# Kernel optimization log

Hardware: AMD Instinct MI355X
Metric: run time of the kernel (lower is better)

## Reference

```python
import jax, jax.numpy as jnp
import numpy as np

N, E = 50000, 1_600_000
IN, HID, OUT = 2048, 64, 64


def setup_inputs() -> dict:
    key = jax.random.key(0)
    k1, k2, k3, k4 = jax.random.split(key, 4)
    x = jax.random.normal(k1, (N, IN), dtype=jnp.float32)
    edge_index = jax.random.randint(k2, (2, E), 0, N, dtype=jnp.int64)
    W1 = jax.random.normal(k3, (IN, HID), dtype=jnp.float32) / np.sqrt(IN)
    b1 = jnp.zeros((HID,), dtype=jnp.float32)
    W2 = jax.random.normal(k4, (HID, OUT), dtype=jnp.float32) / np.sqrt(HID)
    b2 = jnp.zeros((OUT,), dtype=jnp.float32)
    return {"x": x, "edge_index": edge_index, "W1": W1, "b1": b1, "W2": W2, "b2": b2}


def gcn_conv(x, edge_index, W, b):
    # PyG GCNConv: h = XW; out = D^{-1/2} (A + I) D^{-1/2} h + b
    n = x.shape[0]
    h = x @ W  # [n, d_out]
    loops = jnp.arange(n, dtype=edge_index.dtype)
    src = jnp.concatenate([edge_index[0], loops])  # [E+n]
    dst = jnp.concatenate([edge_index[1], loops])
    deg = jax.ops.segment_sum(jnp.ones_like(dst, dtype=h.dtype), dst, num_segments=n)
    dinv = jax.lax.rsqrt(deg)  # deg >= 1 because of self-loops
    norm = dinv[src] * dinv[dst]  # [E+n]
    out = jax.ops.segment_sum(h[src] * norm[:, None], dst, num_segments=n)
    return out + b


def reference(x, edge_index, W1, b1, W2, b2):
    h = jax.nn.relu(gcn_conv(x, edge_index, W1, b1))
    h = jax.nn.relu(gcn_conv(h, edge_index, W2, b2))
    return h.mean(axis=0)  # [OUT]
```

## Files before the change

kernel.cpp:

```cpp
#include <hip/hip_runtime.h>
#include <hip/hip_bf16.h>

typedef __attribute__((ext_vector_type(8))) short short8_t;
typedef __attribute__((ext_vector_type(4))) float f32x4;

__device__ __forceinline__ short f2bf(float x){
  union { float f; unsigned u; } v; v.f = x;
  unsigned r = v.u + 0x7fffu + ((v.u >> 16) & 1u);
  return (short)(r >> 16);
}
__device__ __forceinline__ unsigned pack2(float lo, float hi){
  return (unsigned)(unsigned short)f2bf(lo) | ((unsigned)(unsigned short)f2bf(hi) << 16);
}
__device__ __forceinline__ float bf2f(unsigned short u){
  union { unsigned u; float f; } v; v.u = ((unsigned)u) << 16; return v.f;
}

__global__ __launch_bounds__(256) void k_wconv2(const float* __restrict__ W1, short* __restrict__ Wb1,
                                                const float* __restrict__ W2, short* __restrict__ Wb2){
  int tid = blockIdx.x*256 + threadIdx.x;
  const float* W; short* Wb; int t;
  if (tid < 64*2048){ W = W1; Wb = Wb1; t = tid; }
  else if (tid < 64*2048 + 2*2048){ W = W2; Wb = Wb2; t = tid - 64*2048; }
  else return;
  int e  = t & 7;
  int l  = (t >> 3) & 63;
  int nt = (t >> 9) & 3;
  int kt = t >> 11;
  int k  = kt*32 + (l >> 4)*8 + e;
  int col = nt*16 + (l & 15);
  Wb[t] = f2bf(W[(size_t)k*64 + col]);
}

__global__ __launch_bounds__(256) void k_hist_gemm1(const int* __restrict__ ei, int* __restrict__ cnt,
                                                    int* __restrict__ rank, int E,
                                                    const float* __restrict__ A, const short* __restrict__ Wb,
                                                    float* __restrict__ h1raw, int M, int EB){
  __shared__ unsigned short lds[64*256];
  if ((int)blockIdx.x < EB){
    int i = blockIdx.x*256 + threadIdx.x;
    if (i < E) rank[i] = atomicAdd(&cnt[ei[E + i]], 1);
    return;
  }
  int wid = threadIdx.x >> 6, lane = threadIdx.x & 63;
  int row0 = (blockIdx.x - EB)*64 + wid*16;
  if (row0 >= M) return;
  int rfrag = lane & 15, g = lane >> 4;
  char* ldsb = (char*)lds;
  const short8_t* wb = (const short8_t*)Wb + lane;
  f32x4 acc0 = {0.f,0.f,0.f,0.f}, acc1 = acc0, acc2 = acc0, acc3 = acc0;

  int wbase = wid*16*512;
  int wsel  = (lane >> 1);
  int whalf = (lane & 1) << 3;

  for (int ko = 0; ko < 8; ++ko){
    #pragma unroll
    for (int r = 0; r < 16; ++r){
      const float4 a = *(const float4*)(A + (size_t)(row0 + r)*2048 + ko*256 + lane*4);
      uint2 p; p.x = pack2(a.x, a.y); p.y = pack2(a.z, a.w);
      *(uint2*)(ldsb + wbase + r*512 + ((wsel ^ (r & 7)) << 4) + whalf) = p;
    }
    asm volatile("s_waitcnt lgkmcnt(0)" ::: "memory");
    #pragma unroll
    for (int kt = 0; kt < 8; ++kt){
      short8_t af = *(const short8_t*)(ldsb + wbase + rfrag*512 + ((((kt<<2) + g) ^ (rfrag & 7)) << 4));
      int ktg = ko*8 + kt;
      short8_t b0 = wb[(ktg*4+0)*64];
      short8_t b1 = wb[(ktg*4+1)*64];
      short8_t b2 = wb[(ktg*4+2)*64];
      short8_t b3 = wb[(ktg*4+3)*64];
      acc0 = __builtin_amdgcn_mfma_f32_16x16x32_bf16(af, b0, acc0, 0,0,0);
      acc1 = __builtin_amdgcn_mfma_f32_16x16x32_bf16(af, b1, acc1, 0,0,0);
      acc2 = __builtin_amdgcn_mfma_f32_16x16x32_bf16(af, b2, acc2, 0,0,0);
      acc3 = __builtin_amdgcn_mfma_f32_16x16x32_bf16(af, b3, acc3, 0,0,0);
    }
  }

  int orow = row0 + g*4;
  float* op = h1raw + (size_t)orow*64 + rfrag;
  #pragma unroll
  for (int reg = 0; reg < 4; ++reg){
    op[reg*64 +  0] = acc0[reg];
    op[reg*64 + 16] = acc1[reg];
    op[reg*64 + 32] = acc2[reg];
    op[reg*64 + 48] = acc3[reg];
  }
}

__global__ __launch_bounds__(256) void k_part(const int* __restrict__ cnt, int* __restrict__ partial, int N){
  int b = blockIdx.x, t = threadIdx.x;
  int chunk = (N + 255) >> 8;
  int lo = b*chunk, hi = lo + chunk; if (hi > N) hi = N;
  int s = 0;
  for (int i = lo + t; i < hi; i += 256) s += cnt[i];
  __shared__ int sm[256];
  sm[t] = s; __syncthreads();
  for (int d = 128; d; d >>= 1){ if (t < d) sm[t] += sm[t+d]; __syncthreads(); }
  if (t == 0) partial[b] = sm[0];
}

__global__ __launch_bounds__(256) void k_scan2(const int* __restrict__ cnt, const int* __restrict__ partial,
                                               int* __restrict__ off, float* __restrict__ dinv, int N){
  int b = blockIdx.x, t = threadIdx.x;
  __shared__ int ps[256];
  ps[t] = partial[t]; __syncthreads();
  for (int d = 1; d < 256; d <<= 1){
    int v = (t >= d) ? ps[t-d] : 0; __syncthreads(); ps[t] += v; __syncthreads();
  }
  int base  = b ? ps[b-1] : 0;
  int total = ps[255];
  int chunk = (N + 255) >> 8;
  int lo = b*chunk, hi = lo + chunk; if (hi > N) hi = N;
  __shared__ int vs[256];
  int run = base;
  for (int j0 = lo; j0 < hi; j0 += 256){
    int i = j0 + t;
    int c = (i < hi) ? cnt[i] : 0;
    vs[t] = c; __syncthreads();
    for (int d = 1; d < 256; d <<= 1){
      int v = (t >= d) ? vs[t-d] : 0; __syncthreads(); vs[t] += v; __syncthreads();
    }
    if (i < hi){
      off[i] = run + vs[t] - c;
      dinv[i] = rsqrtf((float)(c + 1));
    }
    run += vs[255];
    __syncthreads();
  }
  if (b == 255 && t == 0) off[N] = total;
}

__global__ __launch_bounds__(256) void k_scatter_scale(const int* __restrict__ ei, const int* __restrict__ off,
                                                       const int* __restrict__ rank, int* __restrict__ ebuf, int E,
                                                       const float* __restrict__ h1raw, const float* __restrict__ dinv,
                                                       unsigned short* __restrict__ h1, int total8, int EB){
  if ((int)blockIdx.x < EB){
    int i = blockIdx.x*256 + threadIdx.x;
    if (i < E){
      int s = ei[i], d = ei[E + i];
      ebuf[off[d] + rank[i]] = s;
    }
    return;
  }
  int t = (blockIdx.x - EB)*256 + threadIdx.x;
  if (t >= total8) return;
  int base = t*8;
  float dv = dinv[base >> 6];
  const float4 a0 = *(const float4*)(h1raw + base);
  const float4 a1 = *(const float4*)(h1raw + base + 4);
  short8_t o;
  o[0]=f2bf(a0.x*dv); o[1]=f2bf(a0.y*dv); o[2]=f2bf(a0.z*dv); o[3]=f2bf(a0.w*dv);
  o[4]=f2bf(a1.x*dv); o[5]=f2bf(a1.y*dv); o[6]=f2bf(a1.z*dv); o[7]=f2bf(a1.w*dv);
  *(short8_t*)(h1 + base) = o;
}

template<int KTILES>
__global__ __launch_bounds__(256) void k_gemm_sm(const unsigned short* __restrict__ Ah,
                                                 const short* __restrict__ Wb, const float* __restrict__ dinv,
                                                 unsigned short* __restrict__ out, int M, int lda){
  int wid = threadIdx.x >> 6, lane = threadIdx.x & 63;
  int row0 = (blockIdx.x*4 + wid)*16;
  if (row0 >= M) return;
  int r = lane & 15, g = lane >> 4;
  const short8_t* wb = (const short8_t*)Wb + lane;
  f32x4 acc0 = {0.f,0.f,0.f,0.f}, acc1 = acc0, acc2 = acc0, acc3 = acc0;
  #pragma unroll
  for (int kt = 0; kt < KTILES; ++kt){
    short8_t af = *(const short8_t*)(Ah + (size_t)(row0 + r)*lda + kt*32 + g*8);
    short8_t b0 = wb[(kt*4+0)*64];
    short8_t b1 = wb[(kt*4+1)*64];
    short8_t b2 = wb[(kt*4+2)*64];
    short8_t b3 = wb[(kt*4+3)*64];
    acc0 = __builtin_amdgcn_mfma_f32_16x16x32_bf16(af, b0, acc0, 0,0,0);
    acc1 = __builtin_amdgcn_mfma_f32_16x16x32_bf16(af, b1, acc1, 0,0,0);
    acc2 = __builtin_amdgcn_mfma_f32_16x16x32_bf16(af, b2, acc2, 0,0,0);
    acc3 = __builtin_amdgcn_mfma_f32_16x16x32_bf16(af, b3, acc3, 0,0,0);
  }
  int orow = row0 + g*4;
  float d0 = dinv[orow], d1 = dinv[orow+1], d2 = dinv[orow+2], d3 = dinv[orow+3];
  unsigned short* op = out + (size_t)orow*64 + r;
  op[0*64 +  0] = (unsigned short)f2bf(acc0[0]*d0);
  op[0*64 + 16] = (unsigned short)f2bf(acc1[0]*d0);
  op[0*64 + 32] = (unsigned short)f2bf(acc2[0]*d0);
  op[0*64 + 48] = (unsigned short)f2bf(acc3[0]*d0);
  op[1*64 +  0] = (unsigned short)f2bf(acc0[1]*d1);
  op[1*64 + 16] = (unsigned short)f2bf(acc1[1]*d1);
  op[1*64 + 32] = (unsigned short)f2bf(acc2[1]*d1);
  op[1*64 + 48] = (unsigned short)f2bf(acc3[1]*d1);
  op[2*64 +  0] = (unsigned short)f2bf(acc0[2]*d2);
  op[2*64 + 16] = (unsigned short)f2bf(acc1[2]*d2);
  op[2*64 + 32] = (unsigned short)f2bf(acc2[2]*d2);
  op[2*64 + 48] = (unsigned short)f2bf(acc3[2]*d2);
  op[3*64 +  0] = (unsigned short)f2bf(acc0[3]*d3);
  op[3*64 + 16] = (unsigned short)f2bf(acc1[3]*d3);
  op[3*64 + 32] = (unsigned short)f2bf(acc2[3]*d3);
  op[3*64 + 48] = (unsigned short)f2bf(acc3[3]*d3);
}

template<bool FUSE>
__global__ __launch_bounds__(256) void k_agg(const unsigned short* __restrict__ hin, const int* __restrict__ off,
                                             const int* __restrict__ ebuf, const float* __restrict__ dinv,
                                             const float* __restrict__ bias, void* __restrict__ outp, int N){
  int lane = threadIdx.x & 63, wid = threadIdx.x >> 6;
  float b = bias[lane];
  float fsum = 0.f;
  int stride = gridDim.x*4;
  for (int i = blockIdx.x*4 + wid; i < N; i += stride){
    float acc = bf2f(hin[(size_t)i*64 + lane]);
    int j  = off[i];
    int j1 = off[i+1];
    for (; j + 4 <= j1; j += 4){
      int s0 = ebuf[j], s1 = ebuf[j+1], s2 = ebuf[j+2], s3 = ebuf[j+3];
      acc += bf2f(hin[(size_t)s0*64 + lane]);
      acc += bf2f(hin[(size_t)s1*64 + lane]);
      acc += bf2f(hin[(size_t)s2*64 + lane]);
      acc += bf2f(hin[(size_t)s3*64 + lane]);
    }
    for (; j < j1; ++j){
      int s = ebuf[j];
      acc += bf2f(hin[(size_t)s*64 + lane]);
    }
    float z = fmaxf(dinv[i]*acc + b, 0.f);
    if (FUSE) fsum += z;
    else ((unsigned short*)outp)[(size_t)i*64 + lane] = (unsigned short)f2bf(z);
  }
  if (FUSE){
    __shared__ float sm[4][64];
    sm[wid][lane] = fsum;
    __syncthreads();
    if (wid == 0)
      ((float*)outp)[(size_t)blockIdx.x*64 + lane] = sm[0][lane] + sm[1][lane] + sm[2][lane] + sm[3][lane];
  }
}

__global__ __launch_bounds__(256) void k_final(const float* __restrict__ part, float* __restrict__ out,
                                               int NB, float invN){
  int f = blockIdx.x;
  float s = 0.f;
  for (int b = threadIdx.x; b < NB; b += 256) s += part[(size_t)b*64 + f];
  __shared__ float sm[256];
  sm[threadIdx.x] = s; __syncthreads();
  for (int d = 128; d > 0; d >>= 1){
    if (threadIdx.x < d) sm[threadIdx.x] += sm[threadIdx.x + d];
    __syncthreads();
  }
  if (threadIdx.x == 0) out[f] = sm[0]*invN;
}

extern "C" void kernel_launch(void* const* d_in, const int* in_sizes, int n_in,
                              void* d_out, int out_size, void* d_ws, size_t ws_size,
                              hipStream_t stream){
  const float* x  = (const float*)d_in[0];
  const int*   ei = (const int*)d_in[1];
  const float* W1 = (const float*)d_in[2];
  const float* b1 = (const float*)d_in[3];
  const float* W2 = (const float*)d_in[4];
  const float* b2 = (const float*)d_in[5];
  float* out = (float*)d_out;

  const int IN = 2048;
  int N = in_sizes[0] / IN;
  int E = in_sizes[1] / 2;

  char* w = (char*)d_ws;
  auto alloc = [&](size_t bytes){ char* p = w; w += (bytes + 255) & ~255ULL; return (void*)p; };
  int*   cnt     = (int*)  alloc((size_t)N*4);
  int*   off     = (int*)  alloc((size_t)(N+1)*4);
  float* dinv    = (float*)alloc((size_t)N*4);
  int*   partial = (int*)  alloc(256*4);
  int*   rank    = (int*)  alloc((size_t)E*4);
  int*   ebuf    = (int*)  alloc((size_t)E*4);
  short* Wb1     = (short*)alloc((size_t)64*2048*2);
  short* Wb2     = (short*)alloc((size_t)2*2048*2);
  float* h1raw   = (float*)alloc((size_t)N*64*4);
  unsigned short* h1 = (unsigned short*)alloc((size_t)N*64*2);
  unsigned short* z1 = (unsigned short*)alloc((size_t)N*64*2);
  const int NB2 = 2048;
  float* part    = (float*)alloc((size_t)NB2*64*4);

  int EB = (E + 255)/256;
  int GB = (N + 63)/64;
  int total8 = N*8;
  int SB = (total8 + 255)/256;
  int smblocks = ((N + 15)/16 + 3)/4;

  hipMemsetAsync(cnt, 0, (size_t)N*4, stream);
  k_wconv2 <<<(64*2048 + 2*2048 + 255)/256, 256, 0, stream>>>(W1, Wb1, W2, Wb2);
  k_hist_gemm1<<<EB + GB, 256, 0, stream>>>(ei, cnt, rank, E, x, Wb1, h1raw, N, EB);
  k_part   <<<256, 256, 0, stream>>>(cnt, partial, N);
  k_scan2  <<<256, 256, 0, stream>>>(cnt, partial, off, dinv, N);
  k_scatter_scale<<<EB + SB, 256, 0, stream>>>(ei, off, rank, ebuf, E, h1raw, dinv, h1, total8, EB);
  k_agg<false><<<NB2, 256, 0, stream>>>(h1, off, ebuf, dinv, b1, (void*)z1, N);
  k_gemm_sm<2><<<smblocks, 256, 0, stream>>>(z1, Wb2, dinv, h1, N, 64);
  k_agg<true> <<<NB2, 256, 0, stream>>>(h1, off, ebuf, dinv, b2, (void*)part, N);
  k_final  <<<64, 256, 0, stream>>>(part, out, NB2, 1.0f/(float)N);
}
```

Before: 366.6 us.

## Split GEMM1 K across wave pairs, interleave histogram blocks, use packed bf16 convert

```diff
diff --git a/kernel.cpp b/kernel.cpp
--- a/kernel.cpp
+++ b/kernel.cpp
@@ -9,8 +9,10 @@
   unsigned r = v.u + 0x7fffu + ((v.u >> 16) & 1u);
   return (short)(r >> 16);
 }
-__device__ __forceinline__ unsigned pack2(float lo, float hi){
-  return (unsigned)(unsigned short)f2bf(lo) | ((unsigned)(unsigned short)f2bf(hi) << 16);
+__device__ __forceinline__ unsigned cvtpk(float lo, float hi){
+  unsigned r;
+  asm volatile("v_cvt_pk_bf16_f32 %0, %1, %2" : "=v"(r) : "v"(lo), "v"(hi));
+  return r;
 }
 __device__ __forceinline__ float bf2f(unsigned short u){
   union { unsigned u; float f; } v; v.u = ((unsigned)u) << 16; return v.f;
@@ -35,17 +37,20 @@
 __global__ __launch_bounds__(256) void k_hist_gemm1(const int* __restrict__ ei, int* __restrict__ cnt,
                                                     int* __restrict__ rank, int E,
                                                     const float* __restrict__ A, const short* __restrict__ Wb,
-                                                    float* __restrict__ h1raw, int M, int EB){
-  __shared__ unsigned short lds[64*256];
-  if ((int)blockIdx.x < EB){
-    int i = blockIdx.x*256 + threadIdx.x;
-    if (i < E) rank[i] = atomicAdd(&cnt[ei[E + i]], 1);
+                                                    float* __restrict__ h1raw, int M, int HB){
+  __shared__ unsigned short lds[4*16*256];
+  int b = blockIdx.x;
+  int tid = threadIdx.x;
+  if (b & 1){
+    for (int i = (b>>1)*256 + tid; i < E; i += HB*256)
+      rank[i] = atomicAdd(&cnt[ei[E + i]], 1);
     return;
   }
-  int wid = threadIdx.x >> 6, lane = threadIdx.x & 63;
-  int row0 = (blockIdx.x - EB)*64 + wid*16;
-  if (row0 >= M) return;
-  int rfrag = lane & 15, g = lane >> 4;
+  int g = b >> 1;
+  int wid = tid >> 6, lane = tid & 63;
+  int tile = wid >> 1, kh = wid & 1;
+  int row0 = g*32 + tile*16;
+  int rfrag = lane & 15, grp = lane >> 4;
   char* ldsb = (char*)lds;
   const short8_t* wb = (const short8_t*)Wb + lane;
   f32x4 acc0 = {0.f,0.f,0.f,0.f}, acc1 = acc0, acc2 = acc0, acc3 = acc0;
@@ -54,18 +59,20 @@
   int wsel  = (lane >> 1);
   int whalf = (lane & 1) << 3;
 
-  for (int ko = 0; ko < 8; ++ko){
+  for (int ko = 0; ko < 4; ++ko){
+    int kcol = kh*1024 + ko*256;
     #pragma unroll
     for (int r = 0; r < 16; ++r){
-      const float4 a = *(const float4*)(A + (size_t)(row0 + r)*2048 + ko*256 + lane*4);
-      uint2 p; p.x = pack2(a.x, a.y); p.y = pack2(a.z, a.w);
+      int rowc = row0 + r; if (rowc >= M) rowc = M - 1;
+      const float4 a = *(const float4*)(A + (size_t)rowc*2048 + kcol + lane*4);
+      uint2 p; p.x = cvtpk(a.x, a.y); p.y = cvtpk(a.z, a.w);
       *(uint2*)(ldsb + wbase + r*512 + ((wsel ^ (r & 7)) << 4) + whalf) = p;
     }
     asm volatile("s_waitcnt lgkmcnt(0)" ::: "memory");
     #pragma unroll
     for (int kt = 0; kt < 8; ++kt){
-      short8_t af = *(const short8_t*)(ldsb + wbase + rfrag*512 + ((((kt<<2) + g) ^ (rfrag & 7)) << 4));
-      int ktg = ko*8 + kt;
+      short8_t af = *(const short8_t*)(ldsb + wbase + rfrag*512 + ((((kt<<2) + grp) ^ (rfrag & 7)) << 4));
+      int ktg = kh*32 + ko*8 + kt;
       short8_t b0 = wb[(ktg*4+0)*64];
       short8_t b1 = wb[(ktg*4+1)*64];
       short8_t b2 = wb[(ktg*4+2)*64];
@@ -77,14 +84,33 @@
     }
   }
 
-  int orow = row0 + g*4;
+  if (kh == 1){
+    float* xch = (float*)(ldsb + wbase);
+    *(f32x4*)(xch + lane*20 +  0) = acc0;
+    *(f32x4*)(xch + lane*20 +  4) = acc1;
+    *(f32x4*)(xch + lane*20 +  8) = acc2;
+    *(f32x4*)(xch + lane*20 + 12) = acc3;
+  }
+  __syncthreads();
+  if (kh == 1) return;
+  {
+    float* px = (float*)(ldsb + (wid+1)*16*512);
+    acc0 += *(const f32x4*)(px + lane*20 +  0);
+    acc1 += *(const f32x4*)(px + lane*20 +  4);
+    acc2 += *(const f32x4*)(px + lane*20 +  8);
+    acc3 += *(const f32x4*)(px + lane*20 + 12);
+  }
+
+  int orow = row0 + grp*4;
   float* op = h1raw + (size_t)orow*64 + rfrag;
   #pragma unroll
   for (int reg = 0; reg < 4; ++reg){
-    op[reg*64 +  0] = acc0[reg];
-    op[reg*64 + 16] = acc1[reg];
-    op[reg*64 + 32] = acc2[reg];
-    op[reg*64 + 48] = acc3[reg];
+    if (orow + reg < M){
+      op[reg*64 +  0] = acc0[reg];
+      op[reg*64 + 16] = acc1[reg];
+      op[reg*64 + 32] = acc2[reg];
+      op[reg*64 + 48] = acc3[reg];
+    }
   }
 }
 
@@ -149,10 +175,10 @@
   float dv = dinv[base >> 6];
   const float4 a0 = *(const float4*)(h1raw + base);
   const float4 a1 = *(const float4*)(h1raw + base + 4);
-  short8_t o;
-  o[0]=f2bf(a0.x*dv); o[1]=f2bf(a0.y*dv); o[2]=f2bf(a0.z*dv); o[3]=f2bf(a0.w*dv);
-  o[4]=f2bf(a1.x*dv); o[5]=f2bf(a1.y*dv); o[6]=f2bf(a1.z*dv); o[7]=f2bf(a1.w*dv);
-  *(short8_t*)(h1 + base) = o;
+  uint2 p0; p0.x = cvtpk(a0.x*dv, a0.y*dv); p0.y = cvtpk(a0.z*dv, a0.w*dv);
+  uint2 p1; p1.x = cvtpk(a1.x*dv, a1.y*dv); p1.y = cvtpk(a1.z*dv, a1.w*dv);
+  uint4 o; o.x = p0.x; o.y = p0.y; o.z = p1.x; o.w = p1.y;
+  *(uint4*)(h1 + base) = o;
 }
 
 template<int KTILES>
@@ -280,14 +306,15 @@
   float* part    = (float*)alloc((size_t)NB2*64*4);
 
   int EB = (E + 255)/256;
-  int GB = (N + 63)/64;
+  int GB = (N + 31)/32;
+  int HB = GB;
   int total8 = N*8;
   int SB = (total8 + 255)/256;
   int smblocks = ((N + 15)/16 + 3)/4;
 
   hipMemsetAsync(cnt, 0, (size_t)N*4, stream);
   k_wconv2 <<<(64*2048 + 2*2048 + 255)/256, 256, 0, stream>>>(W1, Wb1, W2, Wb2);
-  k_hist_gemm1<<<EB + GB, 256, 0, stream>>>(ei, cnt, rank, E, x, Wb1, h1raw, N, EB);
+  k_hist_gemm1<<<2*GB, 256, 0, stream>>>(ei, cnt, rank, E, x, Wb1, h1raw, N, HB);
   k_part   <<<256, 256, 0, stream>>>(cnt, partial, N);
   k_scan2  <<<256, 256, 0, stream>>>(cnt, partial, off, dinv, N);
   k_scatter_scale<<<EB + SB, 256, 0, stream>>>(ei, off, rank, ebuf, E, h1raw, dinv, h1, total8, EB);
```

After: 412.3 us. +12.5%, slower.
